# Kernel tuning notes

Measured on AMD Instinct MI355X. Metric: run time of the kernel, lower is better.

## Reference

```python
import jax, jax.numpy as jnp
import numpy as np

B, S, D = 2, 2048, 1024
H, DH = 16, 64
DM = 4096  # d_mlp = 4*d_model
EPS = 1e-5


def setup_inputs() -> dict:
    key = jax.random.key(0)
    ks = jax.random.split(key, 16)
    s = 0.02
    return {
        "resid_pre": jax.random.normal(ks[0], (B, S, D), jnp.float32),
        "ln1_w": jnp.ones((D,), jnp.float32),
        "ln1_b": jnp.zeros((D,), jnp.float32),
        "W_Q": jax.random.normal(ks[1], (H, D, DH), jnp.float32) * s,
        "W_K": jax.random.normal(ks[2], (H, D, DH), jnp.float32) * s,
        "W_V": jax.random.normal(ks[3], (H, D, DH), jnp.float32) * s,
        "W_O": jax.random.normal(ks[4], (H, DH, D), jnp.float32) * s,
        "b_Q": jnp.zeros((H, DH), jnp.float32),
        "b_K": jnp.zeros((H, DH), jnp.float32),
        "b_V": jnp.zeros((H, DH), jnp.float32),
        "b_O": jnp.zeros((D,), jnp.float32),
        "ln2_w": jnp.ones((D,), jnp.float32),
        "ln2_b": jnp.zeros((D,), jnp.float32),
        "W_in": jax.random.normal(ks[5], (D, DM), jnp.float32) * s,
        "b_in": jnp.zeros((DM,), jnp.float32),
        "W_out": jax.random.normal(ks[6], (DM, D), jnp.float32) * s,
        "b_out": jnp.zeros((D,), jnp.float32),
    }


def _layernorm(x, w, b):
    # TransformerLens LayerNorm: center, scale by sqrt(mean(x^2)+eps), affine
    x = x - x.mean(-1, keepdims=True)
    scale = jnp.sqrt((x * x).mean(-1, keepdims=True) + EPS)
    return x / scale * w + b


def _attention(x, W_Q, W_K, W_V, W_O, b_Q, b_K, b_V, b_O):
    # q,k,v: [batch, pos, head, d_head]
    q = jnp.einsum('bpd,hdk->bphk', x, W_Q) + b_Q
    k = jnp.einsum('bpd,hdk->bphk', x, W_K) + b_K
    v = jnp.einsum('bpd,hdk->bphk', x, W_V) + b_V
    attn_scale = jnp.float32(np.sqrt(DH))
    # scores: [batch, head, query_pos, key_pos]
    scores = jnp.einsum('bqhk,bphk->bhqp', q, k) / attn_scale
    causal = jnp.tril(jnp.ones((S, S), bool))
    scores = jnp.where(causal[None, None, :, :], scores, -jnp.inf)
    pattern = jax.nn.softmax(scores, axis=-1)
    pattern = jnp.where(jnp.isnan(pattern), 0.0, pattern)
    z = jnp.einsum('bphk,bhqp->bqhk', v, pattern)
    return jnp.einsum('bqhk,hkd->bqd', z, W_O) + b_O


def _mlp(x, W_in, b_in, W_out, b_out):
    pre = jnp.einsum('bpd,dm->bpm', x, W_in) + b_in
    post = jax.nn.gelu(pre, approximate=True)  # gelu_new (tanh approx)
    return jnp.einsum('bpm,md->bpd', post, W_out) + b_out


def reference(resid_pre, ln1_w, ln1_b, W_Q, W_K, W_V, W_O, b_Q, b_K, b_V, b_O,
              ln2_w, ln2_b, W_in, b_in, W_out, b_out):
    attn_out = _attention(_layernorm(resid_pre, ln1_w, ln1_b),
                          W_Q, W_K, W_V, W_O, b_Q, b_K, b_V, b_O)
    resid_mid = resid_pre + attn_out
    mlp_out = _mlp(_layernorm(resid_mid, ln2_w, ln2_b), W_in, b_in, W_out, b_out)
    return resid_mid + mlp_out
```

## Files before the change

kernel.cpp:

```cpp
#include <hip/hip_runtime.h>
#include <cstdint>
#include <cstddef>

#define SEQ    2048
#define DMODEL 1024
#define NHEAD  16
#define DHEAD  64
#define DMLP   4096
#define ROWS   4096

typedef __attribute__((ext_vector_type(8))) short bf16x8v;
typedef __attribute__((ext_vector_type(4))) float f32x4;

#define QSCALE 0.18033688011112042f

__device__ __forceinline__ float wave_reduce_sum(float v) {
#pragma unroll
  for (int off = 32; off; off >>= 1) v += __shfl_xor(v, off, 64);
  return v;
}
__device__ __forceinline__ float gelu_new(float x) {
  const float c = 0.7978845608028654f;
  float inner = c * (x + 0.044715f * x * x * x);
  return 0.5f * x * (1.0f + tanhf(inner));
}
__device__ __forceinline__ unsigned short f2bf(float x) {
  union { float f; unsigned u; } v; v.f = x;
  unsigned r = v.u + 0x7fffu + ((v.u >> 16) & 1u);
  return (unsigned short)(r >> 16);
}
__device__ __forceinline__ void gload_lds16(const void* g, void* l) {
  __builtin_amdgcn_global_load_lds(
      (const __attribute__((address_space(1))) unsigned int*)g,
      (__attribute__((address_space(3))) unsigned int*)l, 16, 0, 0);
}

__global__ __launch_bounds__(256)
void ln_bf16_kernel(const float* __restrict__ x, const float* __restrict__ w,
                    const float* __restrict__ b, unsigned short* __restrict__ y) {
  __shared__ float sred[4];
  const int r = blockIdx.x;
  const int t = threadIdx.x;
  const int wid = t >> 6, lane = t & 63;
  const float4 v = ((const float4*)(x + (size_t)r * DMODEL))[t];

  float s = v.x + v.y + v.z + v.w;
  s = wave_reduce_sum(s);
  if (lane == 0) sred[wid] = s;
  __syncthreads();
  const float mean = (sred[0] + sred[1] + sred[2] + sred[3]) * (1.0f / DMODEL);
  __syncthreads();

  float4 c;
  c.x = v.x - mean; c.y = v.y - mean; c.z = v.z - mean; c.w = v.w - mean;
  float ss = c.x * c.x + c.y * c.y + c.z * c.z + c.w * c.w;
  ss = wave_reduce_sum(ss);
  if (lane == 0) sred[wid] = ss;
  __syncthreads();
  const float rs =
      rsqrtf((sred[0] + sred[1] + sred[2] + sred[3]) * (1.0f / DMODEL) + 1e-5f);

  const float4 wv = ((const float4*)w)[t];
  const float4 bv = ((const float4*)b)[t];
  ushort4 o;
  o.x = f2bf(c.x * rs * wv.x + bv.x);
  o.y = f2bf(c.y * rs * wv.y + bv.y);
  o.z = f2bf(c.z * rs * wv.z + bv.z);
  o.w = f2bf(c.w * rs * wv.w + bv.w);
  ((ushort4*)(y + (size_t)r * DMODEL))[t] = o;
}

__global__ __launch_bounds__(256)
void transpose_cvt(const float* __restrict__ src, unsigned short* __restrict__ dst,
                   int ld_src, int ld_dst) {
  __shared__ float t[64][68];
  const int r0 = blockIdx.y * 64, c0 = blockIdx.x * 64;
  const int tid = threadIdx.x;
  const int c4 = (tid & 15) * 4, r = tid >> 4;
#pragma unroll
  for (int p = 0; p < 4; ++p) {
    const float4 v = *(const float4*)(src + (size_t)(r0 + r + p * 16) * ld_src + c0 + c4);
    *(float4*)&t[r + p * 16][c4] = v;
  }
  __syncthreads();
  const int r4 = (tid & 15) * 4, c = tid >> 4;
#pragma unroll
  for (int p = 0; p < 4; ++p) {
    const int cc = c + p * 16;
    ushort4 o;
    o.x = f2bf(t[r4 + 0][cc]);
    o.y = f2bf(t[r4 + 1][cc]);
    o.z = f2bf(t[r4 + 2][cc]);
    o.w = f2bf(t[r4 + 3][cc]);
    *(ushort4*)(dst + (size_t)(c0 + cc) * ld_dst + r0 + r4) = o;
  }
}

__global__ __launch_bounds__(256)
void cvt_wqkv(const float* __restrict__ Wq, const float* __restrict__ Wk,
              const float* __restrict__ Wv, unsigned short* __restrict__ out) {
  __shared__ float t[64][68];
  const float* src = (blockIdx.z == 0) ? Wq : (blockIdx.z == 1) ? Wk : Wv;
  unsigned short* dst = out + (size_t)blockIdx.z * (DMODEL * NHEAD * DHEAD);
  const int h = blockIdx.y, d0 = blockIdx.x * 64;
  const int tid = threadIdx.x;
  const int c4 = (tid & 15) * 4, r = tid >> 4;
#pragma unroll
  for (int p = 0; p < 4; ++p) {
    const float4 v = *(const float4*)(src + (size_t)h * (DMODEL * DHEAD) +
                                      (size_t)(d0 + r + p * 16) * DHEAD + c4);
    *(float4*)&t[r + p * 16][c4] = v;
  }
  __syncthreads();
  const int r4 = (tid & 15) * 4, c = tid >> 4;
#pragma unroll
  for (int p = 0; p < 4; ++p) {
    const int cc = c + p * 16;
    ushort4 o;
    o.x = f2bf(t[r4 + 0][cc]);
    o.y = f2bf(t[r4 + 1][cc]);
    o.z = f2bf(t[r4 + 2][cc]);
    o.w = f2bf(t[r4 + 3][cc]);
    *(ushort4*)(dst + (size_t)(h * 64 + cc) * DMODEL + d0 + r4) = o;
  }
}

template <int EPI>
__global__ __launch_bounds__(256)
void gemm_bf16(const unsigned short* __restrict__ A,
               const unsigned short* __restrict__ Bt,
               const float* __restrict__ bias, const float* __restrict__ addend,
               void* __restrict__ Cout, int ldc, int K) {
  __shared__ unsigned short As[128 * 32];
  __shared__ unsigned short Bs[128 * 32];
  const int tid = threadIdx.x;
  const int w = tid >> 6, lane = tid & 63;
  const int wr = w >> 1, wc = w & 1;
  const int m0 = blockIdx.x * 128, n0 = blockIdx.y * 128;

  f32x4 acc[4][4];
#pragma unroll
  for (int m = 0; m < 4; ++m)
#pragma unroll
    for (int n = 0; n < 4; ++n) acc[m][n] = (f32x4){0.f, 0.f, 0.f, 0.f};

  const int srow = w * 32 + (lane >> 2);
  const int scol = (lane & 3) * 8;

  for (int k0 = 0; k0 < K; k0 += 32) {
    __syncthreads();
#pragma unroll
    for (int it = 0; it < 2; ++it) {
      const int row = srow + it * 16;
      gload_lds16(A + (size_t)(m0 + row) * K + k0 + scol,
                  &As[(w * 32 + it * 16) * 32]);
      gload_lds16(Bt + (size_t)(n0 + row) * K + k0 + scol,
                  &Bs[(w * 32 + it * 16) * 32]);
    }
    __syncthreads();

    bf16x8v af[4], bf[4];
#pragma unroll
    for (int m = 0; m < 4; ++m)
      af[m] = *(const bf16x8v*)&As[(wr * 64 + m * 16 + (lane & 15)) * 32 + (lane >> 4) * 8];
#pragma unroll
    for (int n = 0; n < 4; ++n)
      bf[n] = *(const bf16x8v*)&Bs[(wc * 64 + n * 16 + (lane & 15)) * 32 + (lane >> 4) * 8];
#pragma unroll
    for (int m = 0; m < 4; ++m)
#pragma unroll
      for (int n = 0; n < 4; ++n)
        acc[m][n] = __builtin_amdgcn_mfma_f32_16x16x32_bf16(af[m], bf[n], acc[m][n], 0, 0, 0);
  }

#pragma unroll
  for (int m = 0; m < 4; ++m) {
    const int row = m0 + wr * 64 + m * 16 + (lane >> 4) * 4;
#pragma unroll
    for (int n = 0; n < 4; ++n) {
      const int col = n0 + wc * 64 + n * 16 + (lane & 15);
      const float bcol = bias[col];
      const f32x4 a = acc[m][n];
      if (EPI == 4) {
        ushort4 o;
        o.x = f2bf(a[0] + bcol); o.y = f2bf(a[1] + bcol);
        o.z = f2bf(a[2] + bcol); o.w = f2bf(a[3] + bcol);
        *(ushort4*)((unsigned short*)Cout + (size_t)col * ldc + row) = o;
      } else {
#pragma unroll
        for (int r = 0; r < 4; ++r) {
          const float val = a[r] + bcol;
          const size_t off = (size_t)(row + r) * ldc + col;
          if (EPI == 0) {
            ((float*)Cout)[off] = val;
          } else if (EPI == 1) {
            ((unsigned short*)Cout)[off] = f2bf(gelu_new(val));
          } else if (EPI == 2) {
            ((float*)Cout)[off] = val + addend[off];
          } else if (EPI == 3) {
            ((float*)Cout)[off] += val;
          } else {
            ((unsigned short*)Cout)[off] = f2bf(val);
          }
        }
      }
    }
  }
}

__global__ __launch_bounds__(256)
void gemm_qkv(const unsigned short* __restrict__ A,
              const unsigned short* __restrict__ Bt,
              const float* __restrict__ bQ, const float* __restrict__ bK,
              const float* __restrict__ bV,
              unsigned short* __restrict__ Qb, unsigned short* __restrict__ Kb,
              unsigned short* __restrict__ Vt) {
  __shared__ unsigned short As[128 * 32];
  __shared__ unsigned short Bs[128 * 32];
  const int tid = threadIdx.x;
  const int w = tid >> 6, lane = tid & 63;
  const int wr = w >> 1, wc = w & 1;
  const int m0 = blockIdx.x * 128, n0 = blockIdx.y * 128;

  f32x4 acc[4][4];
#pragma unroll
  for (int m = 0; m < 4; ++m)
#pragma unroll
    for (int n = 0; n < 4; ++n) acc[m][n] = (f32x4){0.f, 0.f, 0.f, 0.f};

  const int srow = w * 32 + (lane >> 2);
  const int scol = (lane & 3) * 8;

  for (int k0 = 0; k0 < DMODEL; k0 += 32) {
    __syncthreads();
#pragma unroll
    for (int it = 0; it < 2; ++it) {
      const int row = srow + it * 16;
      gload_lds16(A + (size_t)(m0 + row) * DMODEL + k0 + scol,
                  &As[(w * 32 + it * 16) * 32]);
      gload_lds16(Bt + (size_t)(n0 + row) * DMODEL + k0 + scol,
                  &Bs[(w * 32 + it * 16) * 32]);
    }
    __syncthreads();

    bf16x8v af[4], bf[4];
#pragma unroll
    for (int m = 0; m < 4; ++m)
      af[m] = *(const bf16x8v*)&As[(wr * 64 + m * 16 + (lane & 15)) * 32 + (lane >> 4) * 8];
#pragma unroll
    for (int n = 0; n < 4; ++n)
      bf[n] = *(const bf16x8v*)&Bs[(wc * 64 + n * 16 + (lane & 15)) * 32 + (lane >> 4) * 8];
#pragma unroll
    for (int m = 0; m < 4; ++m)
#pragma unroll
      for (int n = 0; n < 4; ++n)
        acc[m][n] = __builtin_amdgcn_mfma_f32_16x16x32_bf16(af[m], bf[n], acc[m][n], 0, 0, 0);
  }

  const int which = blockIdx.y >> 3;
  const float* bias = (which == 0) ? bQ : (which == 1) ? bK : bV;
#pragma unroll
  for (int m = 0; m < 4; ++m) {
    const int row = m0 + wr * 64 + m * 16 + (lane >> 4) * 4;
#pragma unroll
    for (int n = 0; n < 4; ++n) {
      const int col = (n0 + wc * 64 + n * 16 + (lane & 15)) & 1023;
      const float bcol = bias[col];
      const f32x4 a = acc[m][n];
      if (which == 2) {
        ushort4 o;
        o.x = f2bf(a[0] + bcol); o.y = f2bf(a[1] + bcol);
        o.z = f2bf(a[2] + bcol); o.w = f2bf(a[3] + bcol);
        *(ushort4*)(Vt + (size_t)col * ROWS + row) = o;
      } else if (which == 1) {
#pragma unroll
        for (int r = 0; r < 4; ++r)
          Kb[(size_t)(row + r) * DMODEL + col] = f2bf(a[r] + bcol);
      } else {
#pragma unroll
        for (int r = 0; r < 4; ++r)
          Qb[(size_t)(row + r) * DMODEL + col] = f2bf((a[r] + bcol) * QSCALE);
      }
    }
  }
}

__global__ __launch_bounds__(512)
void attn_mfma_kernel(const unsigned short* __restrict__ Qb,
                      const unsigned short* __restrict__ Kb,
                      const unsigned short* __restrict__ Vt,
                      unsigned short* __restrict__ Zb) {
  __shared__ unsigned short Ps[8][16][72];
  const int tid = threadIdx.x;
  const int w = tid >> 6, lane = tid & 63;
  const int lg = lane >> 4, lr = lane & 15;
  const int bh = blockIdx.x & 31;
  const int pr = blockIdx.x >> 5;
  const int h = bh & 15, b = bh >> 4;
  const size_t qk_base = (size_t)b * SEQ * DMODEL + (size_t)h * DHEAD;
  const size_t vt_base = (size_t)(h * DHEAD) * ROWS + (size_t)b * SEQ;

  const int qblk = (w < 4) ? pr : (31 - pr);
  const int q0 = qblk * 64 + (w & 3) * 16;
  const int myq = q0 + lr;
  const int jlast = qblk * 64;

  bf16x8v bq[2];
#pragma unroll
  for (int ks = 0; ks < 2; ++ks)
    bq[ks] = *(const bf16x8v*)&Qb[qk_base + (size_t)myq * DMODEL + ks * 32 + lg * 8];

  f32x4 accz[4];
#pragma unroll
  for (int nd = 0; nd < 4; ++nd) accz[nd] = (f32x4){0.f, 0.f, 0.f, 0.f};
  float mq = -3.0e38f, Lq = 0.0f;

  bf16x8v kf[2][4];
#pragma unroll
  for (int ks = 0; ks < 2; ++ks)
#pragma unroll
    for (int n = 0; n < 4; ++n)
      kf[ks][n] = *(const bf16x8v*)
          &Kb[qk_base + (size_t)(n * 16 + lr) * DMODEL + ks * 32 + lg * 8];

  for (int jc = 0; jc <= jlast; jc += 64) {
    f32x4 accs[4];
#pragma unroll
    for (int n = 0; n < 4; ++n) accs[n] = (f32x4){0.f, 0.f, 0.f, 0.f};
#pragma unroll
    for (int ks = 0; ks < 2; ++ks)
#pragma unroll
      for (int n = 0; n < 4; ++n)
        accs[n] = __builtin_amdgcn_mfma_f32_16x16x32_bf16(kf[ks][n], bq[ks], accs[n], 0, 0, 0);

    const int jn = jc + 64;
    if (jn <= jlast) {
#pragma unroll
      for (int ks = 0; ks < 2; ++ks)
#pragma unroll
        for (int n = 0; n < 4; ++n)
          kf[ks][n] = *(const bf16x8v*)
              &Kb[qk_base + (size_t)(jn + n * 16 + lr) * DMODEL + ks * 32 + lg * 8];
    }
    bf16x8v vf[2][4];
#pragma unroll
    for (int ks = 0; ks < 2; ++ks)
#pragma unroll
      for (int nd = 0; nd < 4; ++nd)
        vf[ks][nd] = *(const bf16x8v*)
            &Vt[vt_base + (size_t)(nd * 16 + lr) * ROWS + jc + ks * 32 + lg * 8];

    float mx = -3.0e38f;
    if (jc == jlast) {
#pragma unroll
      for (int n = 0; n < 4; ++n)
#pragma unroll
        for (int r = 0; r < 4; ++r) {
          float s = accs[n][r];
          s = (jc + n * 16 + 4 * lg + r <= myq) ? s : -3.0e38f;
          accs[n][r] = s; mx = fmaxf(mx, s);
        }
    } else {
#pragma unroll
      for (int n = 0; n < 4; ++n)
#pragma unroll
        for (int r = 0; r < 4; ++r) mx = fmaxf(mx, accs[n][r]);
    }
    mx = fmaxf(mx, __shfl_xor(mx, 16, 64));
    mx = fmaxf(mx, __shfl_xor(mx, 32, 64));
    const float mn = fmaxf(mq, mx);
    const float c0 = __builtin_amdgcn_exp2f(mq - mn);
    float sum = 0.0f;
#pragma unroll
    for (int n = 0; n < 4; ++n) {
      ushort4 pk;
      float e0 = __builtin_amdgcn_exp2f(accs[n][0] - mn);
      float e1 = __builtin_amdgcn_exp2f(accs[n][1] - mn);
      float e2 = __builtin_amdgcn_exp2f(accs[n][2] - mn);
      float e3 = __builtin_amdgcn_exp2f(accs[n][3] - mn);
      sum += e0 + e1 + e2 + e3;
      pk.x = f2bf(e0); pk.y = f2bf(e1); pk.z = f2bf(e2); pk.w = f2bf(e3);
      *(ushort4*)&Ps[w][lr][n * 16 + 4 * lg] = pk;
    }
    sum += __shfl_xor(sum, 16, 64);
    sum += __shfl_xor(sum, 32, 64);
    Lq = Lq * c0 + sum;
    mq = mn;
#pragma unroll
    for (int nd = 0; nd < 4; ++nd) accz[nd] *= c0;
    bf16x8v ap[2];
#pragma unroll
    for (int ks = 0; ks < 2; ++ks)
      ap[ks] = *(const bf16x8v*)&Ps[w][lr][ks * 32 + lg * 8];
#pragma unroll
    for (int ks = 0; ks < 2; ++ks)
#pragma unroll
      for (int nd = 0; nd < 4; ++nd)
        accz[nd] = __builtin_amdgcn_mfma_f32_16x16x32_bf16(vf[ks][nd], ap[ks], accz[nd], 0, 0, 0);
  }
  const float rL = 1.0f / Lq;
  unsigned short* zrow = Zb + (size_t)((size_t)b * SEQ + myq) * DMODEL + h * DHEAD;
#pragma unroll
  for (int nd = 0; nd < 4; ++nd) {
    ushort4 o;
    o.x = f2bf(accz[nd][0] * rL);
    o.y = f2bf(accz[nd][1] * rL);
    o.z = f2bf(accz[nd][2] * rL);
    o.w = f2bf(accz[nd][3] * rL);
    *(ushort4*)(zrow + nd * 16 + 4 * lg) = o;
  }
}

extern "C" void kernel_launch(void* const* d_in, const int* in_sizes, int n_in,
                              void* d_out, int out_size, void* d_ws, size_t ws_size,
                              hipStream_t stream) {
  const float* resid_pre = (const float*)d_in[0];
  const float* ln1_w = (const float*)d_in[1];
  const float* ln1_b = (const float*)d_in[2];
  const float* W_Q = (const float*)d_in[3];
  const float* W_K = (const float*)d_in[4];
  const float* W_V = (const float*)d_in[5];
  const float* W_O = (const float*)d_in[6];
  const float* b_Q = (const float*)d_in[7];
  const float* b_K = (const float*)d_in[8];
  const float* b_V = (const float*)d_in[9];
  const float* b_O = (const float*)d_in[10];
  const float* ln2_w = (const float*)d_in[11];
  const float* ln2_b = (const float*)d_in[12];
  const float* W_in = (const float*)d_in[13];
  const float* b_in = (const float*)d_in[14];
  const float* W_out = (const float*)d_in[15];
  const float* b_out = (const float*)d_in[16];
  (void)in_sizes; (void)n_in; (void)out_size; (void)ws_size;

  float* out = (float*)d_out;
  char* w8 = (char*)d_ws;
  unsigned short* xln_b = (unsigned short*)(w8);
  unsigned short* Zb    = (unsigned short*)(w8);
  unsigned short* WQt   = (unsigned short*)(w8 + (8u << 20));
  unsigned short* WOt   = (unsigned short*)(w8 + (14u << 20));
  unsigned short* Wint  = (unsigned short*)(w8 + (16u << 20));
  unsigned short* Woutt = (unsigned short*)(w8 + (24u << 20));
  unsigned short* Qb    = (unsigned short*)(w8 + (32u << 20));
  unsigned short* Kb    = (unsigned short*)(w8 + (40u << 20));
  unsigned short* Vt    = (unsigned short*)(w8 + (48u << 20));
  unsigned short* hid_b = (unsigned short*)(w8 + (32u << 20));

  cvt_wqkv<<<dim3(16, 16, 3), 256, 0, stream>>>(W_Q, W_K, W_V, WQt);
  transpose_cvt<<<dim3(16, 16), 256, 0, stream>>>(W_O, WOt, DMODEL, DMODEL);
  transpose_cvt<<<dim3(64, 16), 256, 0, stream>>>(W_in, Wint, DMLP, DMODEL);
  transpose_cvt<<<dim3(16, 64), 256, 0, stream>>>(W_out, Woutt, DMODEL, DMLP);

  ln_bf16_kernel<<<ROWS, 256, 0, stream>>>(resid_pre, ln1_w, ln1_b, xln_b);
  gemm_qkv<<<dim3(32, 24), 256, 0, stream>>>(xln_b, WQt, b_Q, b_K, b_V, Qb, Kb, Vt);
  attn_mfma_kernel<<<512, 512, 0, stream>>>(Qb, Kb, Vt, Zb);
  dim3 g1024(ROWS / 128, 1024 / 128);
  gemm_bf16<2><<<g1024, 256, 0, stream>>>(Zb, WOt, b_O, resid_pre, out, DMODEL, DMODEL);
  ln_bf16_kernel<<<ROWS, 256, 0, stream>>>(out, ln2_w, ln2_b, xln_b);
  dim3 gin(ROWS / 128, DMLP / 128);
  gemm_bf16<1><<<gin, 256, 0, stream>>>(xln_b, Wint, b_in, nullptr, hid_b, DMLP, DMODEL);
  gemm_bf16<3><<<g1024, 256, 0, stream>>>(hid_b, Woutt, b_out, nullptr, out, DMODEL, DMLP);
}
```

Baseline: 504.1 us.

## Store K and V in MFMA fragment-native layout for contiguous attention loads

The QKV GEMM epilogue now writes K and V per (batch, head) in a pre-swizzled layout that matches the MFMA operand fragments, so each lane's 16-byte load in the attention kernel comes from a contiguous 512-byte block instead of rows strided by DMODEL or ROWS. This is meant to cut the strided, poorly coalesced global reads of K and transposed V inside the attention inner loop. The cost is that the GEMM epilogue for K now does scattered 2-byte stores, and the unused EPI==4 path is dropped from the generic GEMM.

```diff
diff --git a/kernel.cpp b/kernel.cpp
--- a/kernel.cpp
+++ b/kernel.cpp
@@ -181,27 +181,20 @@
       const int col = n0 + wc * 64 + n * 16 + (lane & 15);
       const float bcol = bias[col];
       const f32x4 a = acc[m][n];
-      if (EPI == 4) {
-        ushort4 o;
-        o.x = f2bf(a[0] + bcol); o.y = f2bf(a[1] + bcol);
-        o.z = f2bf(a[2] + bcol); o.w = f2bf(a[3] + bcol);
-        *(ushort4*)((unsigned short*)Cout + (size_t)col * ldc + row) = o;
-      } else {
-#pragma unroll
-        for (int r = 0; r < 4; ++r) {
-          const float val = a[r] + bcol;
-          const size_t off = (size_t)(row + r) * ldc + col;
-          if (EPI == 0) {
-            ((float*)Cout)[off] = val;
-          } else if (EPI == 1) {
-            ((unsigned short*)Cout)[off] = f2bf(gelu_new(val));
-          } else if (EPI == 2) {
-            ((float*)Cout)[off] = val + addend[off];
-          } else if (EPI == 3) {
-            ((float*)Cout)[off] += val;
-          } else {
-            ((unsigned short*)Cout)[off] = f2bf(val);
-          }
+#pragma unroll
+      for (int r = 0; r < 4; ++r) {
+        const float val = a[r] + bcol;
+        const size_t off = (size_t)(row + r) * ldc + col;
+        if (EPI == 0) {
+          ((float*)Cout)[off] = val;
+        } else if (EPI == 1) {
+          ((unsigned short*)Cout)[off] = f2bf(gelu_new(val));
+        } else if (EPI == 2) {
+          ((float*)Cout)[off] = val + addend[off];
+        } else if (EPI == 3) {
+          ((float*)Cout)[off] += val;
+        } else {
+          ((unsigned short*)Cout)[off] = f2bf(val);
         }
       }
     }
@@ -213,8 +206,8 @@
               const unsigned short* __restrict__ Bt,
               const float* __restrict__ bQ, const float* __restrict__ bK,
               const float* __restrict__ bV,
-              unsigned short* __restrict__ Qb, unsigned short* __restrict__ Kb,
-              unsigned short* __restrict__ Vt) {
+              unsigned short* __restrict__ Qb, unsigned short* __restrict__ Kf,
+              unsigned short* __restrict__ Vf) {
   __shared__ unsigned short As[128 * 32];
   __shared__ unsigned short Bs[128 * 32];
   const int tid = threadIdx.x;
@@ -262,24 +255,35 @@
 #pragma unroll
   for (int m = 0; m < 4; ++m) {
     const int row = m0 + wr * 64 + m * 16 + (lane >> 4) * 4;
+    const int bb = row >> 11, s = row & 2047;
 #pragma unroll
     for (int n = 0; n < 4; ++n) {
-      const int col = (n0 + wc * 64 + n * 16 + (lane & 15)) & 1023;
-      const float bcol = bias[col];
+      const int ck = (n0 + wc * 64 + n * 16 + (lane & 15)) & 1023;
+      const float bcol = bias[ck];
       const f32x4 a = acc[m][n];
-      if (which == 2) {
+      if (which == 0) {
+#pragma unroll
+        for (int r = 0; r < 4; ++r)
+          Qb[(size_t)(row + r) * DMODEL + ck] = f2bf((a[r] + bcol) * QSCALE);
+      } else if (which == 1) {
+        const int hh = ck >> 6, dh = ck & 63;
+        const int ks = dh >> 5, lgw = (dh >> 3) & 3, e = dh & 7;
+        const int kc = s >> 6, nf = (s >> 4) & 3, lrw = s & 15;
+        const size_t off = (size_t)(bb * 16 + hh) * (SEQ * DHEAD) +
+                           kc * 4096 + nf * 1024 + ks * 512 + lrw * 32 + lgw * 8 + e;
+#pragma unroll
+        for (int r = 0; r < 4; ++r)
+          Kf[off + r * 32] = f2bf(a[r] + bcol);
+      } else {
+        const int hh = ck >> 6, dh = ck & 63;
+        const int nd = dh >> 4, lrv = dh & 15;
+        const int kc = s >> 6, ks = (s >> 5) & 1, lgw = (s >> 3) & 3, e0 = s & 7;
+        const size_t off = (size_t)(bb * 16 + hh) * (SEQ * DHEAD) +
+                           kc * 4096 + nd * 1024 + ks * 512 + lrv * 32 + lgw * 8 + e0;
         ushort4 o;
         o.x = f2bf(a[0] + bcol); o.y = f2bf(a[1] + bcol);
         o.z = f2bf(a[2] + bcol); o.w = f2bf(a[3] + bcol);
-        *(ushort4*)(Vt + (size_t)col * ROWS + row) = o;
-      } else if (which == 1) {
-#pragma unroll
-        for (int r = 0; r < 4; ++r)
-          Kb[(size_t)(row + r) * DMODEL + col] = f2bf(a[r] + bcol);
-      } else {
-#pragma unroll
-        for (int r = 0; r < 4; ++r)
-          Qb[(size_t)(row + r) * DMODEL + col] = f2bf((a[r] + bcol) * QSCALE);
+        *(ushort4*)&Vf[off] = o;
       }
     }
   }
@@ -287,8 +291,8 @@
 
 __global__ __launch_bounds__(512)
 void attn_mfma_kernel(const unsigned short* __restrict__ Qb,
-                      const unsigned short* __restrict__ Kb,
-                      const unsigned short* __restrict__ Vt,
+                      const unsigned short* __restrict__ Kf,
+                      const unsigned short* __restrict__ Vf,
                       unsigned short* __restrict__ Zb) {
   __shared__ unsigned short Ps[8][16][72];
   const int tid = threadIdx.x;
@@ -297,18 +301,19 @@
   const int bh = blockIdx.x & 31;
   const int pr = blockIdx.x >> 5;
   const int h = bh & 15, b = bh >> 4;
-  const size_t qk_base = (size_t)b * SEQ * DMODEL + (size_t)h * DHEAD;
-  const size_t vt_base = (size_t)(h * DHEAD) * ROWS + (size_t)b * SEQ;
+  const size_t q_base = (size_t)b * SEQ * DMODEL + (size_t)h * DHEAD;
+  const unsigned short* Kfb = Kf + (size_t)bh * (SEQ * DHEAD);
+  const unsigned short* Vfb = Vf + (size_t)bh * (SEQ * DHEAD);
+  const int loff = lr * 32 + lg * 8;
 
   const int qblk = (w < 4) ? pr : (31 - pr);
   const int q0 = qblk * 64 + (w & 3) * 16;
   const int myq = q0 + lr;
-  const int jlast = qblk * 64;
 
   bf16x8v bq[2];
 #pragma unroll
   for (int ks = 0; ks < 2; ++ks)
-    bq[ks] = *(const bf16x8v*)&Qb[qk_base + (size_t)myq * DMODEL + ks * 32 + lg * 8];
+    bq[ks] = *(const bf16x8v*)&Qb[q_base + (size_t)myq * DMODEL + ks * 32 + lg * 8];
 
   f32x4 accz[4];
 #pragma unroll
@@ -320,10 +325,9 @@
   for (int ks = 0; ks < 2; ++ks)
 #pragma unroll
     for (int n = 0; n < 4; ++n)
-      kf[ks][n] = *(const bf16x8v*)
-          &Kb[qk_base + (size_t)(n * 16 + lr) * DMODEL + ks * 32 + lg * 8];
-
-  for (int jc = 0; jc <= jlast; jc += 64) {
+      kf[ks][n] = *(const bf16x8v*)&Kfb[n * 1024 + ks * 512 + loff];
+
+  for (int kc = 0; kc <= qblk; ++kc) {
     f32x4 accs[4];
 #pragma unroll
     for (int n = 0; n < 4; ++n) accs[n] = (f32x4){0.f, 0.f, 0.f, 0.f};
@@ -333,14 +337,13 @@
       for (int n = 0; n < 4; ++n)
         accs[n] = __builtin_amdgcn_mfma_f32_16x16x32_bf16(kf[ks][n], bq[ks], accs[n], 0, 0, 0);
 
-    const int jn = jc + 64;
-    if (jn <= jlast) {
+    if (kc < qblk) {
 #pragma unroll
       for (int ks = 0; ks < 2; ++ks)
 #pragma unroll
         for (int n = 0; n < 4; ++n)
           kf[ks][n] = *(const bf16x8v*)
-              &Kb[qk_base + (size_t)(jn + n * 16 + lr) * DMODEL + ks * 32 + lg * 8];
+              &Kfb[(kc + 1) * 4096 + n * 1024 + ks * 512 + loff];
     }
     bf16x8v vf[2][4];
 #pragma unroll
@@ -348,16 +351,16 @@
 #pragma unroll
       for (int nd = 0; nd < 4; ++nd)
         vf[ks][nd] = *(const bf16x8v*)
-            &Vt[vt_base + (size_t)(nd * 16 + lr) * ROWS + jc + ks * 32 + lg * 8];
+            &Vfb[kc * 4096 + nd * 1024 + ks * 512 + loff];
 
     float mx = -3.0e38f;
-    if (jc == jlast) {
+    if (kc == qblk) {
 #pragma unroll
       for (int n = 0; n < 4; ++n)
 #pragma unroll
         for (int r = 0; r < 4; ++r) {
           float s = accs[n][r];
-          s = (jc + n * 16 + 4 * lg + r <= myq) ? s : -3.0e38f;
+          s = (kc * 64 + n * 16 + 4 * lg + r <= myq) ? s : -3.0e38f;
           accs[n][r] = s; mx = fmaxf(mx, s);
         }
     } else {
@@ -442,8 +445,8 @@
   unsigned short* Wint  = (unsigned short*)(w8 + (16u << 20));
   unsigned short* Woutt = (unsigned short*)(w8 + (24u << 20));
   unsigned short* Qb    = (unsigned short*)(w8 + (32u << 20));
-  unsigned short* Kb    = (unsigned short*)(w8 + (40u << 20));
-  unsigned short* Vt    = (unsigned short*)(w8 + (48u << 20));
+  unsigned short* Kf    = (unsigned short*)(w8 + (40u << 20));
+  unsigned short* Vf    = (unsigned short*)(w8 + (48u << 20));
   unsigned short* hid_b = (unsigned short*)(w8 + (32u << 20));
 
   cvt_wqkv<<<dim3(16, 16, 3), 256, 0, stream>>>(W_Q, W_K, W_V, WQt);
@@ -452,8 +455,8 @@
   transpose_cvt<<<dim3(16, 64), 256, 0, stream>>>(W_out, Woutt, DMODEL, DMLP);
 
   ln_bf16_kernel<<<ROWS, 256, 0, stream>>>(resid_pre, ln1_w, ln1_b, xln_b);
-  gemm_qkv<<<dim3(32, 24), 256, 0, stream>>>(xln_b, WQt, b_Q, b_K, b_V, Qb, Kb, Vt);
-  attn_mfma_kernel<<<512, 512, 0, stream>>>(Qb, Kb, Vt, Zb);
+  gemm_qkv<<<dim3(32, 24), 256, 0, stream>>>(xln_b, WQt, b_Q, b_K, b_V, Qb, Kf, Vf);
+  attn_mfma_kernel<<<512, 512, 0, stream>>>(Qb, Kf, Vf, Zb);
   dim3 g1024(ROWS / 128, 1024 / 128);
   gemm_bf16<2><<<g1024, 256, 0, stream>>>(Zb, WOt, b_O, resid_pre, out, DMODEL, DMODEL);
   ln_bf16_kernel<<<ROWS, 256, 0, stream>>>(out, ln2_w, ln2_b, xln_b);
```

Measured after the change: 445.6 us. 11.6% less time.
